# Kernel tuning notes

Hardware: AMD Instinct MI355X
Metric: run time of the kernel (lower is better)

Reference implementation:

```python
import jax, jax.numpy as jnp
import numpy as np
import math

IMG_SIZE = 768
NUM_CLASSES = 90
THRESHOLD = 0.05
IOU_THRESHOLD = 0.5
MAX_DETECTIONS = 100
K_CAND = 512  # per-class candidate pool before greedy NMS
RATIOS = [(1.0, 1.0), (1.4, 0.7), (0.7, 1.4)]
SCALES = [2 ** 0, 2 ** (1.0 / 3.0), 2 ** (2.0 / 3.0)]


def _generate_anchors():
    anchor_scale = 4.0
    pyramid_levels = [3, 4, 5, 6, 7]
    all_levels = []
    for lv in pyramid_levels:
        stride = 2 ** lv
        size = anchor_scale * 2 ** lv
        grid = IMG_SIZE // stride
        sx = np.arange(grid) * stride
        sy, sx = np.meshgrid(np.arange(grid) * stride, sx, indexing='ij')
        # torch meshgrid(shift_y, shift_x, indexing='ij') -> rows are y
        yy, xx = np.meshgrid(np.arange(grid) * stride, np.arange(grid) * stride, indexing='ij')
        shifts = np.stack([xx.ravel(), yy.ravel(), xx.ravel(), yy.ravel()], axis=1).astype(np.float32)
        base = []
        for r in RATIOS:
            for s in SCALES:
                w = size * s * math.sqrt(r[0] / r[1])
                h = size * s * math.sqrt(r[1] / r[0])
                base.append([-w / 2, -h / 2, w / 2, h / 2])
        base = np.asarray(base, dtype=np.float32)  # [9,4]
        anc = (base[None, :, :] + shifts[:, None, :]).reshape(-1, 4)
        all_levels.append(anc)
    return np.concatenate(all_levels, axis=0)  # [110484,4]


def setup_inputs() -> dict:
    key = jax.random.key(0)
    k1, k2, k3 = jax.random.split(key, 3)
    A = 110484
    x = jax.random.normal(k1, (1, 3, IMG_SIZE, IMG_SIZE), dtype=jnp.float32)
    regression = jax.random.normal(k2, (1, A, 4), dtype=jnp.float32) * 0.3
    classification = jax.random.normal(k3, (1, A, NUM_CLASSES), dtype=jnp.float32) - 2.0
    anchors = jnp.asarray(_generate_anchors())
    return {"x": x, "regression": regression, "classification": classification, "anchors": anchors}


def _decode_and_clip(anchors, deltas, H, W):
    # BBoxTransform (RetinaNet-style): deltas = (dx, dy, dw, dh)
    wa = anchors[:, 2] - anchors[:, 0]
    ha = anchors[:, 3] - anchors[:, 1]
    cxa = anchors[:, 0] + 0.5 * wa
    cya = anchors[:, 1] + 0.5 * ha
    dx, dy, dw, dh = deltas[:, 0], deltas[:, 1], deltas[:, 2], deltas[:, 3]
    cx = cxa + dx * wa
    cy = cya + dy * ha
    w = jnp.exp(dw) * wa
    h = jnp.exp(dh) * ha
    x1 = jnp.clip(cx - 0.5 * w, 0.0, W)
    y1 = jnp.clip(cy - 0.5 * h, 0.0, H)
    x2 = jnp.clip(cx + 0.5 * w, 0.0, W)
    y2 = jnp.clip(cy + 0.5 * h, 0.0, H)
    return jnp.stack([x1, y1, x2, y2], axis=1)  # [A,4]


def _pairwise_iou(b):  # [K,4] -> [K,K]
    area = (b[:, 2] - b[:, 0]) * (b[:, 3] - b[:, 1])
    xx1 = jnp.maximum(b[:, None, 0], b[None, :, 0])
    yy1 = jnp.maximum(b[:, None, 1], b[None, :, 1])
    xx2 = jnp.minimum(b[:, None, 2], b[None, :, 2])
    yy2 = jnp.minimum(b[:, None, 3], b[None, :, 3])
    inter = jnp.clip(xx2 - xx1, 0.0) * jnp.clip(yy2 - yy1, 0.0)
    return inter / (area[:, None] + area[None, :] - inter + 1e-8)


def _greedy_nms(iou_c, valid_c):
    # boxes are pre-sorted by descending score; fixed-iteration greedy NMS
    def step(suppressed, i):
        keep_i = valid_c[i] & jnp.logical_not(suppressed[i])
        suppressed = jnp.where(keep_i, suppressed | (iou_c[i] > IOU_THRESHOLD), suppressed)
        return suppressed, keep_i
    _, keep = jax.lax.scan(step, jnp.zeros(iou_c.shape[0], dtype=bool), jnp.arange(iou_c.shape[0]))
    return keep  # [K]


def _postprocess(x, regression, classification, anchors):
    H, W = x.shape[2], x.shape[3]
    boxes = _decode_and_clip(anchors, regression[0], float(H), float(W))  # [A,4]
    scores = jax.nn.sigmoid(classification[0])                            # [A,C]
    # per-class top-K candidate pool (sorted desc), fixed-shape NMS
    vals, idx = jax.lax.top_k(scores.T, K_CAND)        # [C,K]
    cand = boxes[idx]                                   # [C,K,4]
    valid = vals > THRESHOLD                            # [C,K]
    iou = jax.vmap(_pairwise_iou)(cand)                 # [C,K,K]
    keep = jax.vmap(_greedy_nms)(iou, valid)            # [C,K]
    kept_scores = jnp.where(keep, vals, -1.0).reshape(-1)  # [C*K]
    top_vals, flat_idx = jax.lax.top_k(kept_scores, MAX_DETECTIONS)
    labels = (flat_idx // K_CAND).astype(jnp.float32)
    det_boxes = cand.reshape(-1, 4)[flat_idx]
    ok = top_vals > 0.0
    det = jnp.concatenate([
        jnp.zeros((MAX_DETECTIONS, 1), dtype=jnp.float32),  # batch ids (batch=1 -> 0)
        det_boxes,
        top_vals[:, None],
        labels[:, None],
    ], axis=1)  # [100,7]
    return jnp.where(ok[:, None], det, 0.0)


def reference(x, regression, classification, anchors):
    return _postprocess(x, regression, classification, anchors)
```

## Files before the change

kernel.cpp:

```cpp
#include <hip/hip_runtime.h>
#include <math.h>


#define A_N   110484
#define C_N   90
#define KCAND 512
#define NBINS 8192
#define KSH   19
#define MAXDET 100
#define IMG_F 768.0f
#define THRESH 0.05f
#define NS    4
#define VTOT  (A_N / 4)
#define VS4   ((VTOT + NS - 1) / NS)
#define SL_CAP 1024
#define CAND_N (NS * KCAND)
#define KEEP_CAP 100
#define T_BLKS ((A_N + 63) / 64)
#define S_BLKS (C_N * NS)
#define SEL_T 512
#define D_BLKS ((A_N + SEL_T - 1) / SEL_T)
#define FCAP  512

typedef unsigned int u32;
typedef unsigned long long u64;

__device__ __forceinline__ u32 fkey(float f) {
    u32 u = __float_as_uint(f);
    return (u & 0x80000000u) ? ~u : (u | 0x80000000u);
}
__device__ __forceinline__ float unfkey(u32 k) {
    u32 u = (k & 0x80000000u) ? (k ^ 0x80000000u) : ~k;
    return __uint_as_float(u);
}
__device__ __forceinline__ u64 shflx64(u64 v, int m) {
    u32 lo = (u32)__shfl_xor((int)(u32)v, m, 64);
    u32 hi = (u32)__shfl_xor((int)(v >> 32), m, 64);
    return ((u64)hi << 32) | lo;
}

__global__ __launch_bounds__(256)
void prep_kernel(const float* __restrict__ cls,
                 u32* __restrict__ keysT) {
    __shared__ u32 tile[64 * 91];
    const int a0 = blockIdx.x * 64;
    const int lim = min(64, A_N - a0);
    const int n4 = (lim * C_N) >> 2;
    const float4* src4 = (const float4*)(cls + (size_t)a0 * C_N);
    for (int i4 = threadIdx.x; i4 < n4; i4 += 256) {
        float4 x4 = src4[i4];
        const u32 base = (u32)(4 * i4);
        float xs[4] = { x4.x, x4.y, x4.z, x4.w };
        #pragma unroll
        for (int k = 0; k < 4; ++k) {
            u32 i = base + k;
            u32 aa = i / C_N, c = i % C_N;
            float s = 1.0f / (1.0f + expf(-xs[k]));
            tile[aa * 91 + c] = fkey(s);
        }
    }
    __syncthreads();
    for (int j = threadIdx.x; j < C_N * 64; j += 256) {
        int c = j >> 6, aa = j & 63;
        if (aa < lim)
            keysT[(size_t)c * A_N + a0 + aa] = tile[aa * 91 + c];
    }
}

__global__ __launch_bounds__(SEL_T)
void select_kernel(const u32* __restrict__ keysT,
                   const float* __restrict__ anchors,
                   const float* __restrict__ reg,
                   float4* __restrict__ boxes,
                   u64* __restrict__ candbuf) {
    __shared__ u32 hist[NBINS / 2];
    __shared__ u32 csum[SEL_T];
    __shared__ u64 lbuf[SL_CAP];
    __shared__ u32 sPv;
    __shared__ int lcnt;
    const int tid = threadIdx.x;

    if (blockIdx.x >= S_BLKS) {
        int a = (blockIdx.x - S_BLKS) * SEL_T + tid;
        if (a < A_N) {
            float4 an = ((const float4*)anchors)[a];
            float4 dl = ((const float4*)reg)[a];
            float wa = an.z - an.x, ha = an.w - an.y;
            float cx = an.x + 0.5f * wa + dl.x * wa;
            float cy = an.y + 0.5f * ha + dl.y * ha;
            float w = expf(dl.z) * wa;
            float h = expf(dl.w) * ha;
            float4 o;
            o.x = fminf(fmaxf(cx - 0.5f * w, 0.0f), IMG_F);
            o.y = fminf(fmaxf(cy - 0.5f * h, 0.0f), IMG_F);
            o.z = fminf(fmaxf(cx + 0.5f * w, 0.0f), IMG_F);
            o.w = fminf(fmaxf(cy + 0.5f * h, 0.0f), IMG_F);
            boxes[a] = o;
        }
        return;
    }
    const int c = blockIdx.x >> 2, s = blockIdx.x & 3;
    const int lo = s * VS4, hiEnd = min(VTOT, lo + VS4);
    const uint4* kv = (const uint4*)(keysT + (size_t)c * A_N);

    for (int i = tid; i < NBINS / 2; i += SEL_T) hist[i] = 0;
    if (tid == 0) { sPv = 0; lcnt = 0; }
    __syncthreads();

    #define HACC(K) do { \
        u32 b0 = (K).x >> KSH, b1 = (K).y >> KSH, b2 = (K).z >> KSH, b3 = (K).w >> KSH; \
        atomicAdd(&hist[b0 >> 1], 1u << ((b0 & 1) << 4)); \
        atomicAdd(&hist[b1 >> 1], 1u << ((b1 & 1) << 4)); \
        atomicAdd(&hist[b2 >> 1], 1u << ((b2 & 1) << 4)); \
        atomicAdd(&hist[b3 >> 1], 1u << ((b3 & 1) << 4)); } while (0)
    {
        int i = lo + tid;
        for (; i + 3 * SEL_T < hiEnd; i += 4 * SEL_T) {
            uint4 ka = kv[i], kb = kv[i + SEL_T], kc = kv[i + 2 * SEL_T], kd = kv[i + 3 * SEL_T];
            HACC(ka); HACC(kb); HACC(kc); HACC(kd);
        }
        for (; i < hiEnd; i += SEL_T) { uint4 ka = kv[i]; HACC(ka); }
    }
    __syncthreads();

    u32 own = 0;
    {
        const int wb = (NBINS / 2) - 8 - 8 * tid;
        const int g = (tid >> 2) & 7;
        #pragma unroll
        for (int jj = 0; jj < 8; ++jj) {
            u32 v = hist[wb + ((g + jj) & 7)];
            own += (v & 0xffffu) + (v >> 16);
        }
    }
    csum[tid] = own;
    __syncthreads();
    for (int off = 1; off < SEL_T; off <<= 1) {
        u32 v = csum[tid];
        u32 a = (tid >= off) ? csum[tid - off] : 0u;
        __syncthreads();
        csum[tid] = v + a;
        __syncthreads();
    }
    const u32 incl = csum[tid], excl = incl - own;
    if (excl < (u32)KCAND && incl >= (u32)KCAND) {
        u32 cum = excl;
        const int hb = NBINS - 1 - 16 * tid;
        for (int j = 0; j < 16; ++j) {
            int b = hb - j;
            u32 v = hist[b >> 1];
            u32 cnt = (b & 1) ? (v >> 16) : (v & 0xffffu);
            if (cum + cnt >= (u32)KCAND) { sPv = (u32)b; break; }
            cum += cnt;
        }
    }
    __syncthreads();
    const u32 P = sPv;

    #define CACC(K, BASE) do { \
        if (((K).x >> KSH) >= P) { int p = atomicAdd(&lcnt, 1); if (p < SL_CAP) lbuf[p] = (((u64)(~(K).x)) << 32) | (u32)(BASE); } \
        if (((K).y >> KSH) >= P) { int p = atomicAdd(&lcnt, 1); if (p < SL_CAP) lbuf[p] = (((u64)(~(K).y)) << 32) | (u32)((BASE) + 1); } \
        if (((K).z >> KSH) >= P) { int p = atomicAdd(&lcnt, 1); if (p < SL_CAP) lbuf[p] = (((u64)(~(K).z)) << 32) | (u32)((BASE) + 2); } \
        if (((K).w >> KSH) >= P) { int p = atomicAdd(&lcnt, 1); if (p < SL_CAP) lbuf[p] = (((u64)(~(K).w)) << 32) | (u32)((BASE) + 3); } } while (0)
    {
        int i = lo + tid;
        for (; i + 3 * SEL_T < hiEnd; i += 4 * SEL_T) {
            uint4 ka = kv[i], kb = kv[i + SEL_T], kc = kv[i + 2 * SEL_T], kd = kv[i + 3 * SEL_T];
            CACC(ka, 4 * i); CACC(kb, 4 * (i + SEL_T)); CACC(kc, 4 * (i + 2 * SEL_T)); CACC(kd, 4 * (i + 3 * SEL_T));
        }
        for (; i < hiEnd; i += SEL_T) { uint4 ka = kv[i]; CACC(ka, 4 * i); }
    }
    __syncthreads();
    const int n = min(lcnt, SL_CAP);
    for (int q = tid; q < SL_CAP; q += SEL_T) if (q >= n) lbuf[q] = ~0ULL;
    __syncthreads();

    {
        const int l = tid & 63, w = tid >> 6;
        const int i0 = 128 * w + l, i1 = i0 + 64;
        u64 v0 = lbuf[i0], v1 = lbuf[i1];
        __syncthreads();
        #pragma unroll
        for (u32 kk = 2; kk <= 1024; kk <<= 1) {
            #pragma unroll
            for (u32 j = kk >> 1; j > 0; j >>= 1) {
                if (j >= 128) {
                    lbuf[i0] = v0; lbuf[i1] = v1;
                    __syncthreads();
                    u64 w0 = lbuf[i0 ^ j], w1 = lbuf[i1 ^ j];
                    bool m0 = (((i0 & j) == 0) == ((i0 & kk) == 0));
                    bool m1 = (((i1 & j) == 0) == ((i1 & kk) == 0));
                    v0 = m0 ? (v0 < w0 ? v0 : w0) : (v0 > w0 ? v0 : w0);
                    v1 = m1 ? (v1 < w1 ? v1 : w1) : (v1 > w1 ? v1 : w1);
                    __syncthreads();
                } else if (j == 64) {
                    bool up = ((i0 & kk) == 0);
                    u64 mn = v0 < v1 ? v0 : v1, mx = v0 < v1 ? v1 : v0;
                    v0 = up ? mn : mx; v1 = up ? mx : mn;
                } else {
                    u64 w0 = shflx64(v0, (int)j), w1 = shflx64(v1, (int)j);
                    bool m0 = (((i0 & j) == 0) == ((i0 & kk) == 0));
                    bool m1 = (((i1 & j) == 0) == ((i1 & kk) == 0));
                    v0 = m0 ? (v0 < w0 ? v0 : w0) : (v0 > w0 ? v0 : w0);
                    v1 = m1 ? (v1 < w1 ? v1 : w1) : (v1 > w1 ? v1 : w1);
                }
            }
        }
        if (w < 4) {
            u64* cb = candbuf + (size_t)c * CAND_N + (size_t)s * KCAND;
            const bool rev = (s & 1);
            int d0 = rev ? (KCAND - 1 - i0) : i0;
            int d1 = rev ? (KCAND - 1 - i1) : i1;
            cb[d0] = v0; cb[d1] = v1;
        }
    }
}

__global__ __launch_bounds__(1024, 4)
void nms_kernel(const u64* __restrict__ candbuf,
                const float4* __restrict__ boxes,
                u32* __restrict__ keptbuf, u32* __restrict__ cnt2) {
    __shared__ u64 sortbuf[2][CAND_N];
    __shared__ float4 bb4[KCAND];
    __shared__ float sc[KCAND];
    __shared__ u32 keepf[16], wbase[17];
    u32* bmask = (u32*)&sortbuf[0][0];
    const int c = blockIdx.x, tid = threadIdx.x;
    const int l = tid & 63, w = tid >> 6;
    const int i0 = 128 * w + l, i1 = i0 + 64;

    const u64* cb = candbuf + (size_t)c * CAND_N;
    u64 v0 = cb[i0], v1 = cb[i1];
    int p = 0;
    #pragma unroll
    for (u32 kk = 1024; kk <= (u32)CAND_N; kk <<= 1) {
        #pragma unroll
        for (u32 j = kk >> 1; j > 0; j >>= 1) {
            if (j >= 128) {
                sortbuf[p][i0] = v0; sortbuf[p][i1] = v1;
                __syncthreads();
                u64 w0 = sortbuf[p][i0 ^ j], w1 = sortbuf[p][i1 ^ j];
                bool m0 = (((i0 & j) == 0) == ((i0 & kk) == 0));
                bool m1 = (((i1 & j) == 0) == ((i1 & kk) == 0));
                v0 = m0 ? (v0 < w0 ? v0 : w0) : (v0 > w0 ? v0 : w0);
                v1 = m1 ? (v1 < w1 ? v1 : w1) : (v1 > w1 ? v1 : w1);
                p ^= 1;
            } else if (j == 64) {
                bool up = ((i0 & kk) == 0);
                u64 mn = v0 < v1 ? v0 : v1, mx = v0 < v1 ? v1 : v0;
                v0 = up ? mn : mx; v1 = up ? mx : mn;
            } else {
                u64 w0 = shflx64(v0, (int)j), w1 = shflx64(v1, (int)j);
                bool m0 = (((i0 & j) == 0) == ((i0 & kk) == 0));
                bool m1 = (((i1 & j) == 0) == ((i1 & kk) == 0));
                v0 = m0 ? (v0 < w0 ? v0 : w0) : (v0 > w0 ? v0 : w0);
                v1 = m1 ? (v1 < w1 ? v1 : w1) : (v1 > w1 ? v1 : w1);
            }
        }
    }
    __syncthreads();

    if (w < 4) {
        u32 idx0 = (u32)v0, key0 = ~((u32)(v0 >> 32));
        u32 idx1 = (u32)v1, key1 = ~((u32)(v1 >> 32));
        sc[i0] = unfkey(key0); sc[i1] = unfkey(key1);
        bb4[i0] = boxes[idx0]; bb4[i1] = boxes[idx1];
    }
    if (tid < 16) keepf[tid] = 0;
    __syncthreads();

    {
        const float4 cj0 = bb4[0 * 64 + l], cj1 = bb4[1 * 64 + l];
        const float4 cj2 = bb4[2 * 64 + l], cj3 = bb4[3 * 64 + l];
        const float4 cj4 = bb4[4 * 64 + l], cj5 = bb4[5 * 64 + l];
        const float4 cj6 = bb4[6 * 64 + l], cj7 = bb4[7 * 64 + l];
        const float aj0 = (cj0.z - cj0.x) * (cj0.w - cj0.y);
        const float aj1 = (cj1.z - cj1.x) * (cj1.w - cj1.y);
        const float aj2 = (cj2.z - cj2.x) * (cj2.w - cj2.y);
        const float aj3 = (cj3.z - cj3.x) * (cj3.w - cj3.y);
        const float aj4 = (cj4.z - cj4.x) * (cj4.w - cj4.y);
        const float aj5 = (cj5.z - cj5.x) * (cj5.w - cj5.y);
        const float aj6 = (cj6.z - cj6.x) * (cj6.w - cj6.y);
        const float aj7 = (cj7.z - cj7.x) * (cj7.w - cj7.y);

        #define QSTEP(QQ, CJ, AJ) do { \
            if (QQ >= q0) { \
                float xx1 = fmaxf(bi.x, (CJ).x), yy1 = fmaxf(bi.y, (CJ).y); \
                float xx2 = fminf(bi.z, (CJ).z), yy2 = fminf(bi.w, (CJ).w); \
                float inter = fmaxf(xx2 - xx1, 0.0f) * fmaxf(yy2 - yy1, 0.0f); \
                float uni = ai + (AJ) - inter + 1e-8f; \
                bool sup = ((QQ * 64 + l) > r) && (inter > 0.5f * uni); \
                u64 bal = __ballot(sup); \
                if (l == 0) *(u64*)(row + 2 * QQ) = bal; \
            } } while (0)

        for (int r = w; r < KCAND; r += 16) {
            const float4 bi = bb4[r];
            const float ai = (bi.z - bi.x) * (bi.w - bi.y);
            const int q0 = (r + 1) >> 6;
            u32* row = bmask + r * 16;
            if (l < 2 * q0) row[l] = 0;
            QSTEP(0, cj0, aj0); QSTEP(1, cj1, aj1);
            QSTEP(2, cj2, aj2); QSTEP(3, cj3, aj3);
            QSTEP(4, cj4, aj4); QSTEP(5, cj5, aj5);
            QSTEP(6, cj6, aj6); QSTEP(7, cj7, aj7);
        }
        #undef QSTEP
    }
    __syncthreads();

    if (tid < 64) {
        const int lw = tid & 15;
        u32 removed = 0, keepw = 0;
        u32 rA[8], rB[8]; float sA[8], sB[8];
        #pragma unroll
        for (int k = 0; k < 8; ++k) { rA[k] = bmask[k * 16 + lw]; sA[k] = sc[k]; }
        #pragma unroll 1
        for (int ch = 0; ch < 64; ch += 2) {
            const int tb1 = (ch + 1) * 8;
            #pragma unroll
            for (int k = 0; k < 8; ++k) { rB[k] = bmask[(tb1 + k) * 16 + lw]; sB[k] = sc[tb1 + k]; }
            {
                const int tb = ch * 8;
                #pragma unroll
                for (int k = 0; k < 8; ++k) {
                    const int t = tb + k;
                    u32 rw = (u32)__builtin_amdgcn_readlane((int)removed, t >> 5);
                    bool d = (sA[k] > THRESH) && (((rw >> (t & 31)) & 1u) == 0u);
                    removed |= d ? rA[k] : 0u;
                    keepw |= (d && (tid == (t >> 5))) ? (1u << (t & 31)) : 0u;
                }
            }
            const int tb2 = (ch + 2 < 64) ? (ch + 2) * 8 : 0;
            #pragma unroll
            for (int k = 0; k < 8; ++k) { rA[k] = bmask[(tb2 + k) * 16 + lw]; sA[k] = sc[tb2 + k]; }
            {
                #pragma unroll
                for (int k = 0; k < 8; ++k) {
                    const int t = tb1 + k;
                    u32 rw = (u32)__builtin_amdgcn_readlane((int)removed, t >> 5);
                    bool d = (sB[k] > THRESH) && (((rw >> (t & 31)) & 1u) == 0u);
                    removed |= d ? rB[k] : 0u;
                    keepw |= (d && (tid == (t >> 5))) ? (1u << (t & 31)) : 0u;
                }
            }
            u32 cnt = (u32)__popc(keepw);
            #pragma unroll
            for (int m = 32; m; m >>= 1) cnt += (u32)__shfl_xor((int)cnt, m, 64);
            if (cnt >= (u32)KEEP_CAP) break;
        }
        if (tid < 16) keepf[tid] = keepw;
    }
    __syncthreads();

    if (tid == 0) {
        u32 t = 0;
        for (int q = 0; q < 16; ++q) { wbase[q] = t; t += __popc(keepf[q]); }
        wbase[16] = t;
        cnt2[c] = (t < (u32)KEEP_CAP) ? t : (u32)KEEP_CAP;
    }
    __syncthreads();
    if (tid < KCAND) {
        u32 word = keepf[tid >> 5];
        u32 bit = (u32)tid & 31u;
        if ((word >> bit) & 1u) {
            u32 rank = wbase[tid >> 5] + __popc(word & ((1u << bit) - 1u));
            if (rank < (u32)KEEP_CAP) {
                float s = sc[tid];
                float4 b = bb4[tid];
                uint4 a2, b2;
                a2.x = ~fkey(s);
                a2.y = (u32)(c * KCAND + tid);
                a2.z = __float_as_uint(b.x);
                a2.w = __float_as_uint(b.y);
                b2.x = __float_as_uint(b.z);
                b2.y = __float_as_uint(b.w);
                b2.z = __float_as_uint(s);
                b2.w = 0u;
                uint4* e = (uint4*)(keptbuf + ((size_t)c * KEEP_CAP + rank) * 8);
                e[0] = a2; e[1] = b2;
            }
        }
    }
}

__global__ __launch_bounds__(1024)
void final_kernel(const u32* __restrict__ keptbuf, const u32* __restrict__ cnt2,
                  float* __restrict__ out) {
    __shared__ u32 hist[NBINS];
    __shared__ u32 csum[1024];
    __shared__ u64 ebuf[FCAP];
    __shared__ u32 eidx[FCAP];
    __shared__ u32 scnt[C_N];
    __shared__ u32 sP;
    __shared__ int sN;
    const int tid = threadIdx.x;
    const int TOT = C_N * KEEP_CAP;

    for (int i = tid; i < MAXDET * 7; i += 1024) out[i] = 0.0f;
    for (int i = tid; i < NBINS; i += 1024) hist[i] = 0;
    if (tid < C_N) scnt[tid] = cnt2[tid];
    if (tid == 0) { sN = 0; sP = NBINS - 1; }
    __syncthreads();

    for (int i = tid; i < TOT; i += 1024) {
        u32 c = (u32)i / KEEP_CAP, pp = (u32)i % KEEP_CAP;
        if (pp < scnt[c]) {
            u32 khi = keptbuf[(size_t)i * 8];
            atomicAdd(&hist[khi >> KSH], 1u);
        }
    }
    __syncthreads();
    u32 own = 0; const int lo = 8 * tid;
    #pragma unroll
    for (int j = 0; j < 8; ++j) own += hist[lo + j];
    csum[tid] = own;
    __syncthreads();
    for (int off = 1; off < 1024; off <<= 1) {
        u32 v = csum[tid];
        u32 a = (tid >= off) ? csum[tid - off] : 0u;
        __syncthreads();
        csum[tid] = v + a;
        __syncthreads();
    }
    const u32 incl = csum[tid], excl = incl - own;
    if (excl < (u32)MAXDET && incl >= (u32)MAXDET) {
        u32 cum = excl;
        for (int j = 0; j < 8; ++j) {
            u32 h = hist[lo + j];
            if (cum + h >= (u32)MAXDET) { sP = (u32)(lo + j); break; }
            cum += h;
        }
    }
    __syncthreads();
    const u32 P = sP;
    for (int i = tid; i < TOT; i += 1024) {
        u32 c = (u32)i / KEEP_CAP, pp = (u32)i % KEEP_CAP;
        if (pp < scnt[c]) {
            const uint2 v2 = *((const uint2*)(keptbuf + (size_t)i * 8));
            if ((v2.x >> KSH) <= P) {
                int p = atomicAdd(&sN, 1);
                if (p < FCAP) {
                    ebuf[p] = ((u64)v2.x << 32) | v2.y;
                    eidx[p] = (u32)i;
                }
            }
        }
    }
    __syncthreads();
    const int n = min(sN, FCAP);
    u32 m = 128; while ((int)m < n) m <<= 1;
    for (int i = tid; i < (int)m; i += 1024) if (i >= n) ebuf[i] = ~0ULL;
    __syncthreads();
    for (u32 kk = 2; kk <= m; kk <<= 1) {
        for (u32 j = kk >> 1; j > 0; j >>= 1) {
            u32 i = (u32)tid;
            if (i < m) {
                u32 ixj = i ^ j;
                if (ixj > i) {
                    u64 x = ebuf[i], y = ebuf[ixj];
                    bool up = ((i & kk) == 0);
                    if (up ? (x > y) : (x < y)) {
                        ebuf[i] = y; ebuf[ixj] = x;
                        u32 t = eidx[i]; eidx[i] = eidx[ixj]; eidx[ixj] = t;
                    }
                }
            }
            __syncthreads();
        }
    }
    if (tid < MAXDET && tid < n) {
        u64 comp = ebuf[tid];
        if (comp != ~0ULL) {
            const uint4* e = (const uint4*)(keptbuf + (size_t)eidx[tid] * 8);
            uint4 a = e[0], b = e[1];
            float* o = out + tid * 7;
            o[0] = 0.0f;
            o[1] = __uint_as_float(a.z); o[2] = __uint_as_float(a.w);
            o[3] = __uint_as_float(b.x); o[4] = __uint_as_float(b.y);
            o[5] = __uint_as_float(b.z);
            o[6] = (float)(((u32)comp) >> 9);
        }
    }
}

extern "C" void kernel_launch(void* const* d_in, const int* in_sizes, int n_in,
                              void* d_out, int out_size, void* d_ws, size_t ws_size,
                              hipStream_t stream) {
    const float* reg     = (const float*)d_in[1];
    const float* cls     = (const float*)d_in[2];
    const float* anchors = (const float*)d_in[3];
    float* out = (float*)d_out;

    char* ws = (char*)d_ws;
    size_t off = 0;
    auto alloc = [&](size_t bytes) -> void* {
        void* p = ws + off;
        off = (off + bytes + 255) & ~(size_t)255;
        return p;
    };
    u32*    keysT   = (u32*)   alloc((size_t)C_N * A_N * sizeof(u32));
    float4* boxes   = (float4*)alloc((size_t)A_N * sizeof(float4));
    u64*    candbuf = (u64*)   alloc((size_t)C_N * CAND_N * sizeof(u64));
    u32*    keptbuf = (u32*)   alloc((size_t)C_N * KEEP_CAP * 8 * sizeof(u32));
    u32*    cnt2    = (u32*)   alloc((size_t)C_N * sizeof(u32));
    (void)ws_size;

    prep_kernel<<<T_BLKS, 256, 0, stream>>>(cls, keysT);
    select_kernel<<<S_BLKS + D_BLKS, SEL_T, 0, stream>>>(keysT, anchors, reg, boxes, candbuf);
    nms_kernel<<<C_N, 1024, 0, stream>>>(candbuf, boxes, keptbuf, cnt2);
    final_kernel<<<1, 1024, 0, stream>>>(keptbuf, cnt2, out);
}
```

Before: 184.2 us.

## Select per-class top-K in one block instead of four slices plus merge

The select kernel now uses one block per class that scans the whole class column, instead of four blocks each scanning a quarter. Each block bitonic-sorts up to 2048 survivors (four values per thread) and writes only the top 512. This removes the 2048-element merge sort at the start of the NMS kernel. In exchange the selection phase runs on 90 blocks instead of 360, each doing four times the scanning, which lowers parallelism on a GPU with many compute units. Exceeding the 2048-survivor buffer could also drop candidates.

```diff
diff --git a/kernel.cpp b/kernel.cpp
--- a/kernel.cpp
+++ b/kernel.cpp
@@ -10,14 +10,10 @@
 #define MAXDET 100
 #define IMG_F 768.0f
 #define THRESH 0.05f
-#define NS    4
 #define VTOT  (A_N / 4)
-#define VS4   ((VTOT + NS - 1) / NS)
-#define SL_CAP 1024
-#define CAND_N (NS * KCAND)
+#define SL_CAP 2048
 #define KEEP_CAP 100
 #define T_BLKS ((A_N + 63) / 64)
-#define S_BLKS (C_N * NS)
 #define SEL_T 512
 #define D_BLKS ((A_N + SEL_T - 1) / SEL_T)
 #define FCAP  512
@@ -80,8 +76,8 @@
     __shared__ int lcnt;
     const int tid = threadIdx.x;
 
-    if (blockIdx.x >= S_BLKS) {
-        int a = (blockIdx.x - S_BLKS) * SEL_T + tid;
+    if (blockIdx.x >= C_N) {
+        int a = (blockIdx.x - C_N) * SEL_T + tid;
         if (a < A_N) {
             float4 an = ((const float4*)anchors)[a];
             float4 dl = ((const float4*)reg)[a];
@@ -99,8 +95,7 @@
         }
         return;
     }
-    const int c = blockIdx.x >> 2, s = blockIdx.x & 3;
-    const int lo = s * VS4, hiEnd = min(VTOT, lo + VS4);
+    const int c = blockIdx.x;
     const uint4* kv = (const uint4*)(keysT + (size_t)c * A_N);
 
     for (int i = tid; i < NBINS / 2; i += SEL_T) hist[i] = 0;
@@ -114,12 +109,12 @@
         atomicAdd(&hist[b2 >> 1], 1u << ((b2 & 1) << 4)); \
         atomicAdd(&hist[b3 >> 1], 1u << ((b3 & 1) << 4)); } while (0)
     {
-        int i = lo + tid;
-        for (; i + 3 * SEL_T < hiEnd; i += 4 * SEL_T) {
+        int i = tid;
+        for (; i + 3 * SEL_T < VTOT; i += 4 * SEL_T) {
             uint4 ka = kv[i], kb = kv[i + SEL_T], kc = kv[i + 2 * SEL_T], kd = kv[i + 3 * SEL_T];
             HACC(ka); HACC(kb); HACC(kc); HACC(kd);
         }
-        for (; i < hiEnd; i += SEL_T) { uint4 ka = kv[i]; HACC(ka); }
+        for (; i < VTOT; i += SEL_T) { uint4 ka = kv[i]; HACC(ka); }
     }
     __syncthreads();
 
@@ -163,12 +158,12 @@
         if (((K).z >> KSH) >= P) { int p = atomicAdd(&lcnt, 1); if (p < SL_CAP) lbuf[p] = (((u64)(~(K).z)) << 32) | (u32)((BASE) + 2); } \
         if (((K).w >> KSH) >= P) { int p = atomicAdd(&lcnt, 1); if (p < SL_CAP) lbuf[p] = (((u64)(~(K).w)) << 32) | (u32)((BASE) + 3); } } while (0)
     {
-        int i = lo + tid;
-        for (; i + 3 * SEL_T < hiEnd; i += 4 * SEL_T) {
+        int i = tid;
+        for (; i + 3 * SEL_T < VTOT; i += 4 * SEL_T) {
             uint4 ka = kv[i], kb = kv[i + SEL_T], kc = kv[i + 2 * SEL_T], kd = kv[i + 3 * SEL_T];
             CACC(ka, 4 * i); CACC(kb, 4 * (i + SEL_T)); CACC(kc, 4 * (i + 2 * SEL_T)); CACC(kd, 4 * (i + 3 * SEL_T));
         }
-        for (; i < hiEnd; i += SEL_T) { uint4 ka = kv[i]; CACC(ka, 4 * i); }
+        for (; i < VTOT; i += SEL_T) { uint4 ka = kv[i]; CACC(ka, 4 * i); }
     }
     __syncthreads();
     const int n = min(lcnt, SL_CAP);
@@ -177,42 +172,53 @@
 
     {
         const int l = tid & 63, w = tid >> 6;
-        const int i0 = 128 * w + l, i1 = i0 + 64;
-        u64 v0 = lbuf[i0], v1 = lbuf[i1];
+        int ii[4]; u64 v[4];
+        #pragma unroll
+        for (int r = 0; r < 4; ++r) { ii[r] = 256 * w + 64 * r + l; v[r] = lbuf[ii[r]]; }
         __syncthreads();
         #pragma unroll
-        for (u32 kk = 2; kk <= 1024; kk <<= 1) {
+        for (u32 kk = 2; kk <= (u32)SL_CAP; kk <<= 1) {
             #pragma unroll
             for (u32 j = kk >> 1; j > 0; j >>= 1) {
-                if (j >= 128) {
-                    lbuf[i0] = v0; lbuf[i1] = v1;
+                if (j >= 256) {
+                    #pragma unroll
+                    for (int r = 0; r < 4; ++r) lbuf[ii[r]] = v[r];
                     __syncthreads();
-                    u64 w0 = lbuf[i0 ^ j], w1 = lbuf[i1 ^ j];
-                    bool m0 = (((i0 & j) == 0) == ((i0 & kk) == 0));
-                    bool m1 = (((i1 & j) == 0) == ((i1 & kk) == 0));
-                    v0 = m0 ? (v0 < w0 ? v0 : w0) : (v0 > w0 ? v0 : w0);
-                    v1 = m1 ? (v1 < w1 ? v1 : w1) : (v1 > w1 ? v1 : w1);
+                    #pragma unroll
+                    for (int r = 0; r < 4; ++r) {
+                        u64 pv = lbuf[ii[r] ^ j];
+                        bool up = ((ii[r] & kk) == 0);
+                        bool m = (((ii[r] & j) == 0) == up);
+                        v[r] = m ? (v[r] < pv ? v[r] : pv) : (v[r] > pv ? v[r] : pv);
+                    }
                     __syncthreads();
-                } else if (j == 64) {
-                    bool up = ((i0 & kk) == 0);
-                    u64 mn = v0 < v1 ? v0 : v1, mx = v0 < v1 ? v1 : v0;
-                    v0 = up ? mn : mx; v1 = up ? mx : mn;
+                } else if (j >= 64) {
+                    const int rx = (int)(j >> 6);
+                    u64 nv[4];
+                    #pragma unroll
+                    for (int r = 0; r < 4; ++r) {
+                        u64 pv = v[r ^ rx];
+                        bool up = ((ii[r] & kk) == 0);
+                        bool m = (((ii[r] & j) == 0) == up);
+                        nv[r] = m ? (v[r] < pv ? v[r] : pv) : (v[r] > pv ? v[r] : pv);
+                    }
+                    #pragma unroll
+                    for (int r = 0; r < 4; ++r) v[r] = nv[r];
                 } else {
-                    u64 w0 = shflx64(v0, (int)j), w1 = shflx64(v1, (int)j);
-                    bool m0 = (((i0 & j) == 0) == ((i0 & kk) == 0));
-                    bool m1 = (((i1 & j) == 0) == ((i1 & kk) == 0));
-                    v0 = m0 ? (v0 < w0 ? v0 : w0) : (v0 > w0 ? v0 : w0);
-                    v1 = m1 ? (v1 < w1 ? v1 : w1) : (v1 > w1 ? v1 : w1);
+                    #pragma unroll
+                    for (int r = 0; r < 4; ++r) {
+                        u64 pv = shflx64(v[r], (int)j);
+                        bool up = ((ii[r] & kk) == 0);
+                        bool m = (((ii[r] & j) == 0) == up);
+                        v[r] = m ? (v[r] < pv ? v[r] : pv) : (v[r] > pv ? v[r] : pv);
+                    }
                 }
             }
         }
-        if (w < 4) {
-            u64* cb = candbuf + (size_t)c * CAND_N + (size_t)s * KCAND;
-            const bool rev = (s & 1);
-            int d0 = rev ? (KCAND - 1 - i0) : i0;
-            int d1 = rev ? (KCAND - 1 - i1) : i1;
-            cb[d0] = v0; cb[d1] = v1;
-        }
+        u64* cb = candbuf + (size_t)c * KCAND;
+        #pragma unroll
+        for (int r = 0; r < 4; ++r)
+            if (ii[r] < KCAND) cb[ii[r]] = v[r];
     }
 }
 
@@ -220,51 +226,17 @@
 void nms_kernel(const u64* __restrict__ candbuf,
                 const float4* __restrict__ boxes,
                 u32* __restrict__ keptbuf, u32* __restrict__ cnt2) {
-    __shared__ u64 sortbuf[2][CAND_N];
+    __shared__ u32 bmask[KCAND * 16];
     __shared__ float4 bb4[KCAND];
     __shared__ float sc[KCAND];
     __shared__ u32 keepf[16], wbase[17];
-    u32* bmask = (u32*)&sortbuf[0][0];
     const int c = blockIdx.x, tid = threadIdx.x;
     const int l = tid & 63, w = tid >> 6;
-    const int i0 = 128 * w + l, i1 = i0 + 64;
-
-    const u64* cb = candbuf + (size_t)c * CAND_N;
-    u64 v0 = cb[i0], v1 = cb[i1];
-    int p = 0;
-    #pragma unroll
-    for (u32 kk = 1024; kk <= (u32)CAND_N; kk <<= 1) {
-        #pragma unroll
-        for (u32 j = kk >> 1; j > 0; j >>= 1) {
-            if (j >= 128) {
-                sortbuf[p][i0] = v0; sortbuf[p][i1] = v1;
-                __syncthreads();
-                u64 w0 = sortbuf[p][i0 ^ j], w1 = sortbuf[p][i1 ^ j];
-                bool m0 = (((i0 & j) == 0) == ((i0 & kk) == 0));
-                bool m1 = (((i1 & j) == 0) == ((i1 & kk) == 0));
-                v0 = m0 ? (v0 < w0 ? v0 : w0) : (v0 > w0 ? v0 : w0);
-                v1 = m1 ? (v1 < w1 ? v1 : w1) : (v1 > w1 ? v1 : w1);
-                p ^= 1;
-            } else if (j == 64) {
-                bool up = ((i0 & kk) == 0);
-                u64 mn = v0 < v1 ? v0 : v1, mx = v0 < v1 ? v1 : v0;
-                v0 = up ? mn : mx; v1 = up ? mx : mn;
-            } else {
-                u64 w0 = shflx64(v0, (int)j), w1 = shflx64(v1, (int)j);
-                bool m0 = (((i0 & j) == 0) == ((i0 & kk) == 0));
-                bool m1 = (((i1 & j) == 0) == ((i1 & kk) == 0));
-                v0 = m0 ? (v0 < w0 ? v0 : w0) : (v0 > w0 ? v0 : w0);
-                v1 = m1 ? (v1 < w1 ? v1 : w1) : (v1 > w1 ? v1 : w1);
-            }
-        }
-    }
-    __syncthreads();
-
-    if (w < 4) {
-        u32 idx0 = (u32)v0, key0 = ~((u32)(v0 >> 32));
-        u32 idx1 = (u32)v1, key1 = ~((u32)(v1 >> 32));
-        sc[i0] = unfkey(key0); sc[i1] = unfkey(key1);
-        bb4[i0] = boxes[idx0]; bb4[i1] = boxes[idx1];
+
+    if (tid < KCAND) {
+        u64 e = candbuf[(size_t)c * KCAND + tid];
+        sc[tid] = unfkey(~((u32)(e >> 32)));
+        bb4[tid] = boxes[(u32)e];
     }
     if (tid < 16) keepf[tid] = 0;
     __syncthreads();
@@ -501,13 +473,13 @@
     };
     u32*    keysT   = (u32*)   alloc((size_t)C_N * A_N * sizeof(u32));
     float4* boxes   = (float4*)alloc((size_t)A_N * sizeof(float4));
-    u64*    candbuf = (u64*)   alloc((size_t)C_N * CAND_N * sizeof(u64));
+    u64*    candbuf = (u64*)   alloc((size_t)C_N * KCAND * sizeof(u64));
     u32*    keptbuf = (u32*)   alloc((size_t)C_N * KEEP_CAP * 8 * sizeof(u32));
     u32*    cnt2    = (u32*)   alloc((size_t)C_N * sizeof(u32));
     (void)ws_size;
 
     prep_kernel<<<T_BLKS, 256, 0, stream>>>(cls, keysT);
-    select_kernel<<<S_BLKS + D_BLKS, SEL_T, 0, stream>>>(keysT, anchors, reg, boxes, candbuf);
+    select_kernel<<<C_N + D_BLKS, SEL_T, 0, stream>>>(keysT, anchors, reg, boxes, candbuf);
     nms_kernel<<<C_N, 1024, 0, stream>>>(candbuf, boxes, keptbuf, cnt2);
     final_kernel<<<1, 1024, 0, stream>>>(keptbuf, cnt2, out);
 }
```

After: 204.0 us. 10.7% more time.
